# Kernel tuning notes

Hardware: AMD Instinct MI355X
Metric: run time of the kernel (lower is better)

Reference implementation:

```python
import jax, jax.numpy as jnp
import numpy as np

K = 7          # kernel_size (window)
PAD = (K - 1) // 2  # SAME padding for stride 1


def setup_inputs() -> dict:
    key = jax.random.key(0)
    ks = jax.random.split(key, 7)
    B, H, W, C, F = 8, 128, 128, 256, 256
    rs = F // 2  # rel_size
    return {
        "x": jax.random.normal(ks[0], (B, H, W, C), jnp.float32),
        "Wq": jax.random.normal(ks[1], (C, F), jnp.float32) * 0.05,
        "Wk": jax.random.normal(ks[2], (C, F), jnp.float32) * 0.05,
        "Wv": jax.random.normal(ks[3], (C, F), jnp.float32) * 0.05,
        "rel_x": jax.random.normal(ks[4], (rs, K), jnp.float32) * 0.05,
        "rel_y": jax.random.normal(ks[5], (F - rs, K), jnp.float32) * 0.05,
        "bias": jax.random.normal(ks[6], (1, 1, 1, F), jnp.float32) * (1.0 / np.sqrt(F).astype(np.float32)),
    }


def reference(x, Wq, Wk, Wv, rel_x, rel_y, bias):
    B, H, W, C = x.shape
    rs = rel_x.shape[0]
    # 1x1 conv projections (single group)
    q = jnp.einsum('bhwc,cf->bhwf', x, Wq)
    k = jnp.einsum('bhwc,cf->bhwf', x, Wk)
    v = jnp.einsum('bhwc,cf->bhwf', x, Wv)
    kp = jnp.pad(k, ((0, 0), (PAD, PAD), (PAD, PAD), (0, 0)))
    vp = jnp.pad(v, ((0, 0), (PAD, PAD), (PAD, PAD), (0, 0)))
    # window scores: sum_c q * shifted(k) -> [b,h,w,kh,kw]; avoids im2col blowup
    scores = jnp.stack([
        jnp.stack([jnp.einsum('bhwf,bhwf->bhw', q, kp[:, i:i + H, j:j + W, :])
                   for j in range(K)], axis=-1)
        for i in range(K)], axis=-2)
    # relative position terms: x-half broadcasts along rows (kh), y-half along cols (kw)
    qx = jnp.einsum('bhwx,xk->bhwk', q[..., :rs], rel_x)
    qy = jnp.einsum('bhwy,yk->bhwk', q[..., rs:], rel_y)
    scores = scores + qx[:, :, :, None, :] + qy[:, :, :, :, None]
    attn = jax.nn.softmax(scores.reshape(B, H, W, K * K), axis=-1).reshape(B, H, W, K, K)
    # attention-weighted sum over the window for each channel
    out = sum(attn[:, :, :, i, j][..., None] * vp[:, i:i + H, j:j + W, :]
              for i in range(K) for j in range(K))
    return out + bias
```

## Files before the change

### kernel.cpp

```cpp
#include <hip/hip_runtime.h>
#include <hip/hip_fp16.h>
#include <stdint.h>

typedef _Float16 half8 __attribute__((ext_vector_type(8)));
typedef _Float16 half2v __attribute__((ext_vector_type(2)));
typedef __attribute__((ext_vector_type(4))) float f32x4;

__device__ __forceinline__ unsigned short f2h(float f) {
  __half h = __float2half(f);
  unsigned short u; __builtin_memcpy(&u, &h, 2); return u;
}
__device__ __forceinline__ unsigned pk2h(float a, float b) {
  auto v = __builtin_amdgcn_cvt_pkrtz(a, b);
  unsigned u; __builtin_memcpy(&u, &v, 4); return u;
}
__device__ __forceinline__ half2v h2cast(unsigned u) {
  half2v v; __builtin_memcpy(&v, &u, 4); return v;
}

#if __has_builtin(__builtin_amdgcn_fdot2)
__device__ __forceinline__ float dot2(half2v a, half2v b, float c) {
  return __builtin_amdgcn_fdot2(a, b, c, false);
}
#else
__device__ __forceinline__ float dot2(half2v a, half2v b, float c) {
  return c + (float)a[0] * (float)b[0] + (float)a[1] * (float)b[1];
}
#endif

__device__ __forceinline__ void gl_lds16(const void* g, void* l) {
  __builtin_amdgcn_global_load_lds(
      (const __attribute__((address_space(1))) void*)g,
      (__attribute__((address_space(3))) void*)l, 16, 0, 0);
}

__global__ __launch_bounds__(256) void xcvt(const float* __restrict__ x,
                                            unsigned short* __restrict__ xh) {
  const size_t i = ((size_t)blockIdx.x * 256 + threadIdx.x) * 8;
  float4 a = *(const float4*)&x[i];
  float4 b = *(const float4*)&x[i + 4];
  uint4 o;
  o.x = pk2h(a.x, a.y); o.y = pk2h(a.z, a.w);
  o.z = pk2h(b.x, b.y); o.w = pk2h(b.z, b.w);
  *(uint4*)&xh[i] = o;
}

__global__ __launch_bounds__(256) void wconv(const float* __restrict__ Wq,
                                             const float* __restrict__ Wk,
                                             const float* __restrict__ Wv,
                                             unsigned short* __restrict__ Wb) {
  const int e = blockIdx.x;
  const int w = e >> 8;
  const int n = e & 255;
  const float* W = (w == 0) ? Wq : ((w == 1) ? Wk : Wv);
  const int k = threadIdx.x;
  Wb[(size_t)e * 256 + k] = f2h(W[(size_t)k * 256 + n]);
}

__global__ __launch_bounds__(256) void qkv_gemm(const unsigned short* __restrict__ xh,
                                                const unsigned short* __restrict__ Wb,
                                                unsigned short* __restrict__ qkv) {
  __shared__ unsigned char ldsb[32768];

  const int tid = threadIdx.x;
  const int l = tid & 63, l15 = l & 15, l4 = l >> 4;
  const int wv = tid >> 6, wr = wv >> 1, wc = wv & 1;

  const int pid = blockIdx.x;
  const int cid = (pid & 7) * 768 + (pid >> 3);
  const int by = cid / 6;
  const int bx = cid - by * 6;
  const size_t row0 = (size_t)by * 128;
  const int n0 = bx * 128;

  const int rbase0 = wv * 32, rbase1 = wv * 32 + 16;
  const int rA0 = rbase0 + (l >> 2), rA1 = rbase1 + (l >> 2);
  const int q0 = (l & 3) ^ ((rA0 >> 1) & 3), q1 = (l & 3) ^ ((rA1 >> 1) & 3);
  const unsigned short* gA0 = xh + (row0 + rA0) * 256 + q0 * 8;
  const unsigned short* gA1 = xh + (row0 + rA1) * 256 + q1 * 8;
  const unsigned short* gB0 = Wb + (size_t)(n0 + rA0) * 256 + q0 * 8;
  const unsigned short* gB1 = Wb + (size_t)(n0 + rA1) * 256 + q1 * 8;

  f32x4 acc[4][4] = {};

  auto stage = [&](int s, int d) {
    gl_lds16(gA0 + s * 32, &ldsb[d * 8192 + rbase0 * 64]);
    gl_lds16(gA1 + s * 32, &ldsb[d * 8192 + rbase1 * 64]);
    gl_lds16(gB0 + s * 32, &ldsb[16384 + d * 8192 + rbase0 * 64]);
    gl_lds16(gB1 + s * 32, &ldsb[16384 + d * 8192 + rbase1 * 64]);
  };

  stage(0, 0);
  __syncthreads();

  for (int s = 0; s < 8; ++s) {
    const int d = s & 1;
    if (s < 7) stage(s + 1, d ^ 1);
    half8 af[4], bf[4];
#pragma unroll
    for (int m = 0; m < 4; ++m) {
      const int r = wr * 64 + m * 16 + l15;
      af[m] = *(const half8*)&ldsb[d * 8192 + r * 64 + ((l4 ^ ((r >> 1) & 3)) * 16)];
    }
#pragma unroll
    for (int n = 0; n < 4; ++n) {
      const int r = wc * 64 + n * 16 + l15;
      bf[n] = *(const half8*)&ldsb[16384 + d * 8192 + r * 64 + ((l4 ^ ((r >> 1) & 3)) * 16)];
    }
#pragma unroll
    for (int n = 0; n < 4; ++n)
#pragma unroll
      for (int m = 0; m < 4; ++m)
        acc[m][n] = __builtin_amdgcn_mfma_f32_16x16x32_f16(af[m], bf[n], acc[m][n], 0, 0, 0);
    __syncthreads();
  }

#pragma unroll
  for (int m = 0; m < 4; ++m)
#pragma unroll
    for (int n = 0; n < 4; ++n) {
      const int ng = n0 + wc * 64 + n * 16 + l15;
      unsigned short* op = qkv + (size_t)(ng >> 8) * 33554432 + (ng & 255);
#pragma unroll
      for (int r = 0; r < 4; ++r) {
        const size_t grow = row0 + wr * 64 + m * 16 + l4 * 4 + r;
        op[grow * 256] = f2h(acc[m][n][r]);
      }
    }
}

__global__ __launch_bounds__(256) void qrel(const unsigned short* __restrict__ q,
                                            const float* __restrict__ relx,
                                            const float* __restrict__ rely,
                                            unsigned short* __restrict__ qr) {
  __shared__ unsigned wpk[896];
  for (int i = threadIdx.x; i < 896; i += 256) {
    const int hf = (i >= 448) ? 1 : 0;
    const int r = i - hf * 448;
    const int c2 = r / 7, j = r - c2 * 7;
    const float* R = hf ? rely : relx;
    wpk[i] = pk2h(R[(2 * c2) * 7 + j], R[(2 * c2 + 1) * 7 + j]);
  }
  __syncthreads();
  const size_t pix = (size_t)blockIdx.x * 256 + threadIdx.x;
  const uint4* qp = (const uint4*)(q + pix * 256);
  float ax[7] = {0, 0, 0, 0, 0, 0, 0}, ay[7] = {0, 0, 0, 0, 0, 0, 0};
#pragma unroll
  for (int g = 0; g < 32; ++g) {
    const uint4 u = qp[g];
    const int c2b = (g & 15) * 4;
    if (g < 16) {
#pragma unroll
      for (int j = 0; j < 7; ++j) {
        float s = ax[j];
        s = dot2(h2cast(u.x), h2cast(wpk[(c2b + 0) * 7 + j]), s);
        s = dot2(h2cast(u.y), h2cast(wpk[(c2b + 1) * 7 + j]), s);
        s = dot2(h2cast(u.z), h2cast(wpk[(c2b + 2) * 7 + j]), s);
        s = dot2(h2cast(u.w), h2cast(wpk[(c2b + 3) * 7 + j]), s);
        ax[j] = s;
      }
    } else {
#pragma unroll
      for (int j = 0; j < 7; ++j) {
        float s = ay[j];
        s = dot2(h2cast(u.x), h2cast(wpk[448 + (c2b + 0) * 7 + j]), s);
        s = dot2(h2cast(u.y), h2cast(wpk[448 + (c2b + 1) * 7 + j]), s);
        s = dot2(h2cast(u.z), h2cast(wpk[448 + (c2b + 2) * 7 + j]), s);
        s = dot2(h2cast(u.w), h2cast(wpk[448 + (c2b + 3) * 7 + j]), s);
        ay[j] = s;
      }
    }
  }
  uint4 o0, o1;
  o0.x = pk2h(ax[0], ax[1]); o0.y = pk2h(ax[2], ax[3]);
  o0.z = pk2h(ax[4], ax[5]); o0.w = pk2h(ax[6], ay[0]);
  o1.x = pk2h(ay[1], ay[2]); o1.y = pk2h(ay[3], ay[4]);
  o1.z = pk2h(ay[5], ay[6]); o1.w = 0;
  uint4* dst = (uint4*)(qr + pix * 512);
  dst[0] = o0; dst[1] = o1;
}

__global__ __launch_bounds__(256) void attn(const unsigned short* __restrict__ qkv,
                                            const float* __restrict__ bias,
                                            const unsigned short* __restrict__ qrelb,
                                            float* __restrict__ out) {
  __shared__ unsigned short kv[2][4][4256];

  const int tid = threadIdx.x;
  const int col = tid & 31, row = tid >> 5;
  const int wv = tid >> 6;
  const int l = tid & 63, lo = l & 15, hi = l >> 4;

  const int pid = blockIdx.x;
  const int cid = (pid & 7) * 64 + (pid >> 3);
  const int ht = cid & 15, wt = (cid >> 4) & 3, b = cid >> 6;

  const int h = ht * 8 + row, w = wt * 32 + col;
  const size_t pix = (size_t)((b * 128 + h) * 128 + w);
  const int pbase = row * 38 + col;

  const unsigned short* qb = qkv;
  const unsigned short* kb = qkv + 33554432;
  const unsigned short* vb = qkv + 67108864;

  const int pr0 = tid / 38, pc0 = tid - pr0 * 38;
  const int gh0 = ht * 8 + pr0 - 3, gw0 = wt * 32 + pc0 - 3;
  const bool ok0 = ((unsigned)gh0 < 128u) && ((unsigned)gw0 < 128u);
  const long long go0 = ((long long)((b * 128 + gh0) * 128 + gw0)) * 256;

  const int p1 = tid + 256;
  const int pr1 = p1 / 38, pc1 = p1 - pr1 * 38;
  const int gh1 = ht * 8 + pr1 - 3, gw1 = wt * 32 + pc1 - 3;
  const bool ok1 = ((unsigned)gh1 < 128u) && ((unsigned)gw1 < 128u);
  const long long go1 = ((long long)((b * 128 + gh1) * 128 + gw1)) * 256;

  const int p2 = tid + 512;
  const int pr2 = p2 / 38, pc2 = p2 - pr2 * 38;
  const int gh2 = ht * 8 + pr2 - 3, gw2 = wt * 32 + pc2 - 3;
  const bool ok2 = (p2 < 532) && ((unsigned)gh2 < 128u) && ((unsigned)gw2 < 128u);
  const long long go2 = ((long long)((b * 128 + gh2) * 128 + gw2)) * 256;

  const int wb8 = wv * 512;

  auto stage = [&](const unsigned short* base, int c, int d) {
#pragma unroll
    for (int g = 0; g < 4; ++g) {
      if (ok0) gl_lds16(base + go0 + c * 32 + g * 8, &kv[d][g][wb8]);
      if (ok1) gl_lds16(base + go1 + c * 32 + g * 8, &kv[d][g][2048 + wb8]);
      if (ok2) gl_lds16(base + go2 + c * 32 + g * 8, &kv[d][g][4096]);
    }
  };

  auto zero_oob = [&]() {
    const uint4 z = make_uint4(0u, 0u, 0u, 0u);
    for (int p = tid; p < 532; p += 256) {
      const int pr = p / 38, pc = p - pr * 38;
      const int gh = ht * 8 + pr - 3, gw = wt * 32 + pc - 3;
      if (!((unsigned)gh < 128u && (unsigned)gw < 128u)) {
#pragma unroll
        for (int d = 0; d < 2; ++d)
#pragma unroll
          for (int g = 0; g < 4; ++g)
            *(uint4*)&kv[d][g][p * 8] = z;
      }
    }
  };

  zero_oob();
  stage(kb, 0, 0);
  __syncthreads();

  int slot0[7];
#pragma unroll
  for (int t = 0; t < 7; ++t) {
    const int p = t * 16 + lo;
    const int ur = p / 14, uc = p - ur * 14;
    slot0[t] = (2 * wv + ur) * 38 + uc;
  }
  const size_t qpix = (size_t)((b * 128 + ht * 8 + 2 * wv + (lo >> 3)) * 128 + wt * 32 + (lo & 7));
  const unsigned short* qlane = qb + qpix * 256 + hi * 8;

  f32x4 acc[4][7] = {};

  for (int s = 0; s < 8; ++s) {
    const int d = s & 1;
    if (s < 7) stage(kb, s + 1, d ^ 1);
    half8 qf[4];
#pragma unroll
    for (int g = 0; g < 4; ++g)
      qf[g] = *(const half8*)(qlane + (size_t)g * 2048 + s * 32);
    const unsigned short* kpl = &kv[d][hi][0];
    __builtin_amdgcn_s_setprio(1);
#pragma unroll
    for (int t = 0; t < 7; ++t) {
      const unsigned short* kt = kpl + slot0[t] * 8;
#pragma unroll
      for (int g = 0; g < 4; ++g) {
        const half8 kf = *(const half8*)(kt + g * 64);
        acc[g][t] = __builtin_amdgcn_mfma_f32_16x16x32_f16(qf[g], kf, acc[g][t], 0, 0, 0);
      }
    }
    __builtin_amdgcn_s_setprio(0);
    __syncthreads();
  }

  float* pbuf = (float*)&kv[0][0][0];
#pragma unroll
  for (int t = 0; t < 7; ++t) {
    const int p = t * 16 + lo;
    const int ur = p / 14, uc = p - ur * 14;
#pragma unroll
    for (int r = 0; r < 4; ++r) {
      const int qq = hi * 4 + r;
      const int di = ur - (qq >> 3), dj = uc - (qq & 7);
      if (((unsigned)di < 7u) && ((unsigned)dj < 7u)) {
        const int prow_ = wv * 64 + (qq >> 3) * 32 + (qq & 7);
        const int pslot = di * 7 + dj;
#pragma unroll
        for (int g = 0; g < 4; ++g)
          pbuf[(prow_ + g * 8) * 52 + pslot] = acc[g][t][r];
      }
    }
  }
  __syncthreads();

  float sc[49];
  {
    const float* prow = pbuf + tid * 52;
#pragma unroll
    for (int k = 0; k < 12; ++k) {
      const float4 v = ((const float4*)prow)[k];
      sc[k * 4 + 0] = v.x; sc[k * 4 + 1] = v.y;
      sc[k * 4 + 2] = v.z; sc[k * 4 + 3] = v.w;
    }
    sc[48] = prow[48];
  }
  __syncthreads();

  zero_oob();
  stage(vb, 0, 0);

  float qx[7], qy[7];
  {
    const uint4* rp = (const uint4*)(qrelb + pix * 512);
    uint4 r0 = rp[0], r1 = rp[1];
    half2v a0 = h2cast(r0.x), a1 = h2cast(r0.y), a2 = h2cast(r0.z), a3 = h2cast(r0.w);
    half2v b0 = h2cast(r1.x), b1 = h2cast(r1.y), b2 = h2cast(r1.z);
    qx[0] = a0[0]; qx[1] = a0[1]; qx[2] = a1[0]; qx[3] = a1[1];
    qx[4] = a2[0]; qx[5] = a2[1]; qx[6] = a3[0];
    qy[0] = a3[1]; qy[1] = b0[0]; qy[2] = b0[1]; qy[3] = b1[0];
    qy[4] = b1[1]; qy[5] = b2[0]; qy[6] = b2[1];
  }

#pragma unroll
  for (int i = 0; i < 7; ++i)
#pragma unroll
    for (int j = 0; j < 7; ++j) sc[i * 7 + j] += qx[j] + qy[i];
  float mx = sc[0];
#pragma unroll
  for (int t = 1; t < 49; ++t) mx = fmaxf(mx, sc[t]);
  float sum = 0.0f;
#pragma unroll
  for (int t = 0; t < 49; ++t) {
    float e = __expf(sc[t] - mx);
    sc[t] = e;
    sum += e;
  }
  const float invs = 1.0f / sum;
  unsigned pw[49];
#pragma unroll
  for (int t = 0; t < 49; ++t) {
    const unsigned short ph = f2h(sc[t] * invs);
    pw[t] = (unsigned)ph | ((unsigned)ph << 16);
  }
  __syncthreads();

  for (int s = 0; s < 8; ++s) {
    const int d = s & 1;
    const int f0 = s * 32;
    if (s < 7) stage(vb, s + 1, d ^ 1);
    half2v acc2[16];
#pragma unroll
    for (int a = 0; a < 16; ++a) acc2[a] = half2v{(_Float16)0, (_Float16)0};
    __builtin_amdgcn_s_setprio(1);
#pragma unroll
    for (int i = 0; i < 7; ++i)
#pragma unroll
      for (int j = 0; j < 7; ++j) {
        const int q8 = (pbase + i * 38 + j) * 8;
        uint4 v0 = *(const uint4*)&kv[d][0][q8];
        uint4 v1 = *(const uint4*)&kv[d][1][q8];
        uint4 v2 = *(const uint4*)&kv[d][2][q8];
        uint4 v3 = *(const uint4*)&kv[d][3][q8];
        const half2v p2h = h2cast(pw[i * 7 + j]);
        acc2[0] += p2h * h2cast(v0.x);  acc2[1] += p2h * h2cast(v0.y);
        acc2[2] += p2h * h2cast(v0.z);  acc2[3] += p2h * h2cast(v0.w);
        acc2[4] += p2h * h2cast(v1.x);  acc2[5] += p2h * h2cast(v1.y);
        acc2[6] += p2h * h2cast(v1.z);  acc2[7] += p2h * h2cast(v1.w);
        acc2[8] += p2h * h2cast(v2.x);  acc2[9] += p2h * h2cast(v2.y);
        acc2[10] += p2h * h2cast(v2.z); acc2[11] += p2h * h2cast(v2.w);
        acc2[12] += p2h * h2cast(v3.x); acc2[13] += p2h * h2cast(v3.y);
        acc2[14] += p2h * h2cast(v3.z); acc2[15] += p2h * h2cast(v3.w);
      }
    __builtin_amdgcn_s_setprio(0);
#pragma unroll
    for (int fq = 0; fq < 8; ++fq) {
      float4 bv = *(const float4*)&bias[f0 + fq * 4];
      float4 o;
      o.x = (float)acc2[fq * 2 + 0][0] + bv.x;
      o.y = (float)acc2[fq * 2 + 0][1] + bv.y;
      o.z = (float)acc2[fq * 2 + 1][0] + bv.z;
      o.w = (float)acc2[fq * 2 + 1][1] + bv.w;
      *(float4*)&out[pix * 256 + f0 + fq * 4] = o;
    }
    if (s < 7) __syncthreads();
  }
}

extern "C" void kernel_launch(void* const* d_in, const int* in_sizes, int n_in,
                              void* d_out, int out_size, void* d_ws, size_t ws_size,
                              hipStream_t stream) {
  const float* x = (const float*)d_in[0];
  const float* Wq = (const float*)d_in[1];
  const float* Wk = (const float*)d_in[2];
  const float* Wv = (const float*)d_in[3];
  const float* relx = (const float*)d_in[4];
  const float* rely = (const float*)d_in[5];
  const float* bias = (const float*)d_in[6];
  float* out = (float*)d_out;

  unsigned short* xh = (unsigned short*)d_out;
  unsigned short* qrl = (unsigned short*)d_out;
  unsigned short* Wb = (unsigned short*)d_ws;
  unsigned short* qkv = (unsigned short*)((char*)d_ws + 393216);

  xcvt<<<dim3(16384), dim3(256), 0, stream>>>(x, xh);
  wconv<<<dim3(768), dim3(256), 0, stream>>>(Wq, Wk, Wv, Wb);
  qkv_gemm<<<dim3(6144), dim3(256), 0, stream>>>(xh, Wb, qkv);
  qrel<<<dim3(512), dim3(256), 0, stream>>>(qkv, relx, rely, qrl);
  attn<<<dim3(512), dim3(256), 0, stream>>>(qkv, bias, qrl, out);
}
```

Baseline: 300.4 us.

## Double attention block threads to 512, splitting channels and pixel columns across waves

The attention kernel now launches 512 threads per block instead of 256. In the QK MFMA phase each wave handles half the pixel columns (16 instead of 32), and in the PV phase each thread handles half the channels of each 32-channel chunk. This halves per-thread accumulator registers and gives more waves to hide LDS and global latency, at the cost of some duplicated softmax work per pixel (two threads per pixel) and more barrier participants.

```diff
diff --git a/kernel.cpp b/kernel.cpp
--- a/kernel.cpp
+++ b/kernel.cpp
@@ -180,16 +180,20 @@
   dst[0] = o0; dst[1] = o1;
 }
 
-__global__ __launch_bounds__(256) void attn(const unsigned short* __restrict__ qkv,
-                                            const float* __restrict__ bias,
-                                            const unsigned short* __restrict__ qrelb,
-                                            float* __restrict__ out) {
+__global__ __launch_bounds__(512, 2) void attn(const unsigned short* __restrict__ qkv,
+                                               const float* __restrict__ bias,
+                                               const unsigned short* __restrict__ qrelb,
+                                               float* __restrict__ out) {
   __shared__ unsigned short kv[2][4][4256];
 
   const int tid = threadIdx.x;
-  const int col = tid & 31, row = tid >> 5;
+  const int px = tid & 255;
+  const int ph = tid >> 8;
+  const int col = px & 31, row = px >> 5;
   const int wv = tid >> 6;
-  const int l = tid & 63, lo = l & 15, hi = l >> 4;
+  const int lo = tid & 15, hi = (tid >> 4) & 3;
+  const int rp = wv >> 1;
+  const int ch16 = (wv & 1) * 16;
 
   const int pid = blockIdx.x;
   const int cid = (pid & 7) * 64 + (pid >> 3);
@@ -208,32 +212,23 @@
   const bool ok0 = ((unsigned)gh0 < 128u) && ((unsigned)gw0 < 128u);
   const long long go0 = ((long long)((b * 128 + gh0) * 128 + gw0)) * 256;
 
-  const int p1 = tid + 256;
+  const int p1 = tid + 512;
   const int pr1 = p1 / 38, pc1 = p1 - pr1 * 38;
   const int gh1 = ht * 8 + pr1 - 3, gw1 = wt * 32 + pc1 - 3;
-  const bool ok1 = ((unsigned)gh1 < 128u) && ((unsigned)gw1 < 128u);
+  const bool ok1 = (p1 < 532) && ((unsigned)gh1 < 128u) && ((unsigned)gw1 < 128u);
   const long long go1 = ((long long)((b * 128 + gh1) * 128 + gw1)) * 256;
 
-  const int p2 = tid + 512;
-  const int pr2 = p2 / 38, pc2 = p2 - pr2 * 38;
-  const int gh2 = ht * 8 + pr2 - 3, gw2 = wt * 32 + pc2 - 3;
-  const bool ok2 = (p2 < 532) && ((unsigned)gh2 < 128u) && ((unsigned)gw2 < 128u);
-  const long long go2 = ((long long)((b * 128 + gh2) * 128 + gw2)) * 256;
-
-  const int wb8 = wv * 512;
-
   auto stage = [&](const unsigned short* base, int c, int d) {
 #pragma unroll
     for (int g = 0; g < 4; ++g) {
-      if (ok0) gl_lds16(base + go0 + c * 32 + g * 8, &kv[d][g][wb8]);
-      if (ok1) gl_lds16(base + go1 + c * 32 + g * 8, &kv[d][g][2048 + wb8]);
-      if (ok2) gl_lds16(base + go2 + c * 32 + g * 8, &kv[d][g][4096]);
+      if (ok0) gl_lds16(base + go0 + c * 32 + g * 8, &kv[d][g][wv * 512]);
+      if (ok1) gl_lds16(base + go1 + c * 32 + g * 8, &kv[d][g][4096]);
     }
   };
 
   auto zero_oob = [&]() {
     const uint4 z = make_uint4(0u, 0u, 0u, 0u);
-    for (int p = tid; p < 532; p += 256) {
+    for (int p = tid; p < 532; p += 512) {
       const int pr = p / 38, pc = p - pr * 38;
       const int gh = ht * 8 + pr - 3, gw = wt * 32 + pc - 3;
       if (!((unsigned)gh < 128u && (unsigned)gw < 128u)) {
@@ -255,19 +250,20 @@
   for (int t = 0; t < 7; ++t) {
     const int p = t * 16 + lo;
     const int ur = p / 14, uc = p - ur * 14;
-    slot0[t] = (2 * wv + ur) * 38 + uc;
-  }
-  const size_t qpix = (size_t)((b * 128 + ht * 8 + 2 * wv + (lo >> 3)) * 128 + wt * 32 + (lo & 7));
+    slot0[t] = (2 * rp + ur) * 38 + ch16 + uc;
+  }
+  const size_t qpix =
+      (size_t)((b * 128 + ht * 8 + 2 * rp + (lo >> 3)) * 128 + wt * 32 + ch16 + (lo & 7));
   const unsigned short* qlane = qb + qpix * 256 + hi * 8;
 
-  f32x4 acc[4][7] = {};
+  f32x4 acc[2][7] = {};
 
   for (int s = 0; s < 8; ++s) {
     const int d = s & 1;
     if (s < 7) stage(kb, s + 1, d ^ 1);
-    half8 qf[4];
-#pragma unroll
-    for (int g = 0; g < 4; ++g)
+    half8 qf[2];
+#pragma unroll
+    for (int g = 0; g < 2; ++g)
       qf[g] = *(const half8*)(qlane + (size_t)g * 2048 + s * 32);
     const unsigned short* kpl = &kv[d][hi][0];
     __builtin_amdgcn_s_setprio(1);
@@ -275,7 +271,7 @@
     for (int t = 0; t < 7; ++t) {
       const unsigned short* kt = kpl + slot0[t] * 8;
 #pragma unroll
-      for (int g = 0; g < 4; ++g) {
+      for (int g = 0; g < 2; ++g) {
         const half8 kf = *(const half8*)(kt + g * 64);
         acc[g][t] = __builtin_amdgcn_mfma_f32_16x16x32_f16(qf[g], kf, acc[g][t], 0, 0, 0);
       }
@@ -291,14 +287,15 @@
     const int ur = p / 14, uc = p - ur * 14;
 #pragma unroll
     for (int r = 0; r < 4; ++r) {
-      const int qq = hi * 4 + r;
-      const int di = ur - (qq >> 3), dj = uc - (qq & 7);
+      const int q = hi * 4 + r;
+      const int di = ur - (q >> 3), dj = uc - (q & 7);
       if (((unsigned)di < 7u) && ((unsigned)dj < 7u)) {
-        const int prow_ = wv * 64 + (qq >> 3) * 32 + (qq & 7);
         const int pslot = di * 7 + dj;
 #pragma unroll
-        for (int g = 0; g < 4; ++g)
-          pbuf[(prow_ + g * 8) * 52 + pslot] = acc[g][t][r];
+        for (int g = 0; g < 2; ++g) {
+          const int prow_ = (2 * rp + (q >> 3)) * 32 + ch16 + 8 * g + (q & 7);
+          pbuf[prow_ * 52 + pslot] = acc[g][t][r];
+        }
       }
     }
   }
@@ -306,7 +303,7 @@
 
   float sc[49];
   {
-    const float* prow = pbuf + tid * 52;
+    const float* prow = pbuf + px * 52;
 #pragma unroll
     for (int k = 0; k < 12; ++k) {
       const float4 v = ((const float4*)prow)[k];
@@ -322,8 +319,8 @@
 
   float qx[7], qy[7];
   {
-    const uint4* rp = (const uint4*)(qrelb + pix * 512);
-    uint4 r0 = rp[0], r1 = rp[1];
+    const uint4* rpq = (const uint4*)(qrelb + pix * 512);
+    uint4 r0 = rpq[0], r1 = rpq[1];
     half2v a0 = h2cast(r0.x), a1 = h2cast(r0.y), a2 = h2cast(r0.z), a3 = h2cast(r0.w);
     half2v b0 = h2cast(r1.x), b1 = h2cast(r1.y), b2 = h2cast(r1.z);
     qx[0] = a0[0]; qx[1] = a0[1]; qx[2] = a1[0]; qx[3] = a1[1];
@@ -350,41 +347,35 @@
   unsigned pw[49];
 #pragma unroll
   for (int t = 0; t < 49; ++t) {
-    const unsigned short ph = f2h(sc[t] * invs);
-    pw[t] = (unsigned)ph | ((unsigned)ph << 16);
+    const unsigned short phv = f2h(sc[t] * invs);
+    pw[t] = (unsigned)phv | ((unsigned)phv << 16);
   }
   __syncthreads();
 
   for (int s = 0; s < 8; ++s) {
     const int d = s & 1;
-    const int f0 = s * 32;
+    const int f0 = s * 32 + ph * 16;
     if (s < 7) stage(vb, s + 1, d ^ 1);
-    half2v acc2[16];
-#pragma unroll
-    for (int a = 0; a < 16; ++a) acc2[a] = half2v{(_Float16)0, (_Float16)0};
+    half2v acc2[8];
+#pragma unroll
+    for (int a = 0; a < 8; ++a) acc2[a] = half2v{(_Float16)0, (_Float16)0};
     __builtin_amdgcn_s_setprio(1);
 #pragma unroll
     for (int i = 0; i < 7; ++i)
 #pragma unroll
       for (int j = 0; j < 7; ++j) {
         const int q8 = (pbase + i * 38 + j) * 8;
-        uint4 v0 = *(const uint4*)&kv[d][0][q8];
-        uint4 v1 = *(const uint4*)&kv[d][1][q8];
-        uint4 v2 = *(const uint4*)&kv[d][2][q8];
-        uint4 v3 = *(const uint4*)&kv[d][3][q8];
+        uint4 v0 = *(const uint4*)&kv[d][2 * ph + 0][q8];
+        uint4 v1 = *(const uint4*)&kv[d][2 * ph + 1][q8];
         const half2v p2h = h2cast(pw[i * 7 + j]);
         acc2[0] += p2h * h2cast(v0.x);  acc2[1] += p2h * h2cast(v0.y);
         acc2[2] += p2h * h2cast(v0.z);  acc2[3] += p2h * h2cast(v0.w);
         acc2[4] += p2h * h2cast(v1.x);  acc2[5] += p2h * h2cast(v1.y);
         acc2[6] += p2h * h2cast(v1.z);  acc2[7] += p2h * h2cast(v1.w);
-        acc2[8] += p2h * h2cast(v2.x);  acc2[9] += p2h * h2cast(v2.y);
-        acc2[10] += p2h * h2cast(v2.z); acc2[11] += p2h * h2cast(v2.w);
-        acc2[12] += p2h * h2cast(v3.x); acc2[13] += p2h * h2cast(v3.y);
-        acc2[14] += p2h * h2cast(v3.z); acc2[15] += p2h * h2cast(v3.w);
       }
     __builtin_amdgcn_s_setprio(0);
 #pragma unroll
-    for (int fq = 0; fq < 8; ++fq) {
+    for (int fq = 0; fq < 4; ++fq) {
       float4 bv = *(const float4*)&bias[f0 + fq * 4];
       float4 o;
       o.x = (float)acc2[fq * 2 + 0][0] + bv.x;
@@ -418,5 +409,5 @@
   wconv<<<dim3(768), dim3(256), 0, stream>>>(Wq, Wk, Wv, Wb);
   qkv_gemm<<<dim3(6144), dim3(256), 0, stream>>>(xh, Wb, qkv);
   qrel<<<dim3(512), dim3(256), 0, stream>>>(qkv, relx, rely, qrl);
-  attn<<<dim3(512), dim3(256), 0, stream>>>(qkv, bias, qrl, out);
-}
+  attn<<<dim3(512), dim3(512), 0, stream>>>(qkv, bias, qrl, out);
+}
```

Result: faster. 282.7 us (-5.9%).
